# Optimization experiments

Hardware: AMD Instinct MI355X
Metric: run time of the kernel (lower is better)

## Reference

```python
import jax, jax.numpy as jnp
import numpy as np

NEG_SLOPE = 0.01  # jax.nn.leaky_relu default

def bicubic_resize(x, target_h, target_w):
    # NHWC bicubic resize with antialiasing (matches original module)
    b, h, w, c = x.shape
    return jax.image.resize(x, shape=(b, target_h, target_w, c), method='bicubic', antialias=True)

def setup_inputs() -> dict:
    key = jax.random.key(0)
    x = jax.random.normal(key, (16, 128, 128, 128), dtype=jnp.float32)  # NHWC
    return {"x": x, "in_size": 128, "out_size": 128}

def reference(x, in_size, out_size):
    y = bicubic_resize(x, 2 * in_size, 2 * in_size)
    # activation on the fine grid
    y = jax.nn.leaky_relu(y, negative_slope=NEG_SLOPE)
    # downsample (antialiased) back to out_size
    y = bicubic_resize(y, out_size, out_size)
    return y
```

## Files before the change

### kernel.cpp

```cpp
#include <hip/hip_runtime.h>


typedef float f2 __attribute__((ext_vector_type(2)));

#define HH 128
#define WW 128
#define CC 128
#define RS 16
#define CH 16
#define PADF2 130
#define NSTEP (RS + 4)

#define LBAR() asm volatile("s_waitcnt lgkmcnt(0)\n\ts_barrier" ::: "memory")

__device__ __forceinline__ double keys_cubic(double x) {
  if (x >= 2.0) return 0.0;
  if (x >= 1.0) return ((-0.5 * x + 2.5) * x - 4.0) * x + 2.0;
  return (1.5 * x - 2.5) * x * x + 1.0;
}

__global__ __launch_bounds__(256) void fused_updown_kernel(
    const float* __restrict__ x, float* __restrict__ out) {
  __shared__ __align__(16) float wUpV[256][4];
  __shared__ __align__(16) float wDnE[4][8];
  __shared__ __align__(16) f2 rowv[2][CH][PADF2];

  const int tid = threadIdx.x;

  {
    const int k = tid;
    const double q = 0.5 * k - 0.25;
    const int st = ((k + 1) >> 1) - 2;
    double wr[4], s = 0.0;
#pragma unroll
    for (int i = 0; i < 4; ++i) {
      const int col = st + i;
      double w = (col >= 0 && col <= 127) ? keys_cubic(fabs((double)col - q)) : 0.0;
      wr[i] = w; s += w;
    }
    const double inv = 1.0 / s;
#pragma unroll
    for (int i = 0; i < 4; ++i) wUpV[k][i] = (float)(wr[i] * inv);
  }
  if (tid < 4) {
    const int e = tid;
    const int j = (e < 2) ? e : 124 + e;
    const double p = 2.0 * j + 0.5;
    const int st = 2 * j - 3;
    double wr[8], s = 0.0;
#pragma unroll
    for (int i = 0; i < 8; ++i) {
      const int col = st + i;
      double w = (col >= 0 && col <= 255) ? keys_cubic(0.5 * fabs((double)col - p)) : 0.0;
      wr[i] = w; s += w;
    }
    const double inv = 1.0 / s;
#pragma unroll
    for (int i = 0; i < 8; ++i) wDnE[e][i] = (float)(wr[i] * inv);
  }
  __syncthreads();

  const int bid = blockIdx.x;
  const int b = bid & 15;
  const int strip = (bid >> 4) & 7;
  const int chunk = bid >> 7;
  const int oy0 = strip * RS;
  const int c0 = chunk * CH;
  const int c = tid & 15;
  const int g = tid >> 4;
  const int col0 = g * 8;
  const bool gL = (g == 0), gR = (g == 15);

  const float* xbase = x + (size_t)b * (HH * WW * CC) + (size_t)col0 * CC + (c0 + c);
  float* obase = out + (size_t)b * (HH * WW * CC) + (size_t)col0 * CC + (c0 + c);
  const int m0 = oy0 - 2;

  auto load_row = [&](float (&d)[8], int row) {
    row = row < 0 ? 0 : (row > 127 ? 127 : row);
    const float* p = xbase + (size_t)row * (WW * CC);
#pragma unroll
    for (int j = 0; j < 8; ++j) d[j] = p[j * CC];
  };

  auto wdGet = [&](int oy, float cst, int tap) -> float {
    if (oy < 0 || oy > 127) return 0.f;
    if (oy < 2) return wDnE[oy][tap];
    if (oy > 125) return wDnE[oy - 124][tap];
    return cst;
  };

  float r0[8], r1[8], r2[8], r3[8], r4[8], r5[8];
  float A0[8], A1[8], A2[8], A3[8], A4[8];
#pragma unroll
  for (int i = 0; i < 8; ++i) { A0[i]=0.f; A1[i]=0.f; A2[i]=0.f; A3[i]=0.f; A4[i]=0.f; }

  load_row(r0, m0 - 2);
  load_row(r1, m0 - 1);
  load_row(r2, m0);
  load_row(r3, m0 + 1);
  load_row(r4, m0 + 2);
  load_row(r5, m0 + 3);

  for (int t = 0; t < NSTEP; ++t) {
    const int m = m0 + t;
    if (t > 0) {
#pragma unroll
      for (int i = 0; i < 8; ++i) {
        r0[i]=r1[i]; r1[i]=r2[i]; r2[i]=r3[i]; r3[i]=r4[i]; r4[i]=r5[i];
      }
      load_row(r5, m + 3);
    }
    const bool mOK = (m >= 0) && (m <= 127);
    const int sp = t & 1;
    f2 vown[8];
    if (mOK) {
      float4 we, wo;
      if (m >= 2 && m <= 125) {
        we = make_float4(-0.0234375f, 0.2265625f, 0.8671875f, -0.0703125f);
        wo = make_float4(-0.0703125f, 0.8671875f, 0.2265625f, -0.0234375f);
      } else {
        we = *(const float4*)wUpV[2 * m];
        wo = *(const float4*)wUpV[2 * m + 1];
      }
#pragma unroll
      for (int j = 0; j < 8; ++j) {
        vown[j].x = (we.x * r0[j] + we.y * r1[j]) + (we.z * r2[j] + we.w * r3[j]);
        vown[j].y = (wo.x * r1[j] + wo.y * r2[j]) + (wo.z * r3[j] + wo.w * r4[j]);
      }
#pragma unroll
      for (int j = 0; j < 8; ++j) rowv[sp][c][col0 + j] = vown[j];
    }
    LBAR();
    if (mOK) {
      f2 vv[16];
      if (!gL) {
#pragma unroll
        for (int i = 0; i < 4; ++i) vv[i] = rowv[sp][c][col0 - 4 + i];
      } else {
#pragma unroll
        for (int i = 0; i < 4; ++i) vv[i] = f2{0.f, 0.f};
      }
#pragma unroll
      for (int j = 0; j < 8; ++j) vv[4 + j] = vown[j];
      if (!gR) {
#pragma unroll
        for (int i = 0; i < 4; ++i) vv[12 + i] = rowv[sp][c][col0 + 8 + i];
      } else {
#pragma unroll
        for (int i = 0; i < 4; ++i) vv[12 + i] = f2{0.f, 0.f};
      }

      f2 ff[22];
#pragma unroll
      for (int u = 0; u < 22; ++u) {
        const int s = (u >> 1) + 1;
        f2 t2;
        if (u & 1)
          t2 = (vv[s] * (-0.0234375f) + vv[s + 1] * 0.2265625f)
             + (vv[s + 2] * 0.8671875f + vv[s + 3] * (-0.0703125f));
        else
          t2 = (vv[s] * (-0.0703125f) + vv[s + 1] * 0.8671875f)
             + (vv[s + 2] * 0.2265625f + vv[s + 3] * (-0.0234375f));
        ff[u] = __builtin_elementwise_max(t2, t2 * 0.01f);
      }
      if (gL) {
#pragma unroll
        for (int u = 3; u <= 5; ++u) {
          const int s = (u >> 1) + 1;
          const float4 w = *(const float4*)wUpV[u - 3];
          f2 t2 = (vv[s] * w.x + vv[s + 1] * w.y) + (vv[s + 2] * w.z + vv[s + 3] * w.w);
          ff[u] = __builtin_elementwise_max(t2, t2 * 0.01f);
        }
      }
      if (gR) {
#pragma unroll
        for (int u = 16; u <= 18; ++u) {
          const int s = (u >> 1) + 1;
          const float4 w = *(const float4*)wUpV[237 + u];
          f2 t2 = (vv[s] * w.x + vv[s + 1] * w.y) + (vv[s + 2] * w.z + vv[s + 3] * w.w);
          ff[u] = __builtin_elementwise_max(t2, t2 * 0.01f);
        }
      }

      f2 tt[8];
#pragma unroll
      for (int jj = 0; jj < 8; ++jj) {
        const f2 p0 = ff[2*jj]     + ff[2*jj + 7];
        const f2 p1 = ff[2*jj + 1] + ff[2*jj + 6];
        const f2 p2 = ff[2*jj + 2] + ff[2*jj + 5];
        const f2 p3 = ff[2*jj + 3] + ff[2*jj + 4];
        tt[jj] = (p0 * (-0.01171875f) + p1 * (-0.03515625f))
               + (p2 * 0.11328125f    + p3 * 0.43359375f);
      }
      if (gL) {
#pragma unroll
        for (int jj = 0; jj < 2; ++jj) {
          f2 s2 = f2{0.f, 0.f};
#pragma unroll
          for (int i = 0; i < 8; ++i) s2 += ff[2*jj + i] * wDnE[jj][i];
          tt[jj] = s2;
        }
      }
      if (gR) {
#pragma unroll
        for (int jj = 6; jj < 8; ++jj) {
          f2 s2 = f2{0.f, 0.f};
#pragma unroll
          for (int i = 0; i < 8; ++i) s2 += ff[2*jj + i] * wDnE[jj - 4][i];
          tt[jj] = s2;
        }
      }

      const float wE0 = wdGet(m - 2, -0.01171875f, 7);
      const float wE1 = wdGet(m - 1, 0.11328125f, 5);
      const float wE2 = wdGet(m, 0.43359375f, 3);
      const float wE3 = wdGet(m + 1, -0.03515625f, 1);
      const float wO0 = wdGet(m - 1, -0.03515625f, 6);
      const float wO1 = wdGet(m, 0.43359375f, 4);
      const float wO2 = wdGet(m + 1, 0.11328125f, 2);
      const float wO3 = wdGet(m + 2, -0.01171875f, 0);
#pragma unroll
      for (int jj = 0; jj < 8; ++jj) {
        const float te = tt[jj].x, to = tt[jj].y;
        A0[jj] = fmaf(wE0, te, A0[jj]);
        A1[jj] = fmaf(wE1, te, fmaf(wO0, to, A1[jj]));
        A2[jj] = fmaf(wE2, te, fmaf(wO1, to, A2[jj]));
        A3[jj] = fmaf(wE3, te, fmaf(wO2, to, A3[jj]));
        A4[jj] = fmaf(wO3, to, A4[jj]);
      }
    }
    if (m - 2 >= oy0) {
      float* op = obase + (size_t)(m - 2) * (WW * CC);
#pragma unroll
      for (int jj = 0; jj < 8; ++jj) op[jj * CC] = A0[jj];
    }
#pragma unroll
    for (int jj = 0; jj < 8; ++jj) {
      A0[jj]=A1[jj]; A1[jj]=A2[jj]; A2[jj]=A3[jj]; A3[jj]=A4[jj]; A4[jj]=0.f;
    }
  }
}

extern "C" void kernel_launch(void* const* d_in, const int* in_sizes, int n_in,
                              void* d_out, int out_size, void* d_ws, size_t ws_size,
                              hipStream_t stream) {
  const float* x = (const float*)d_in[0];
  float* o = (float*)d_out;
  dim3 grid(16 * 8 * 8);
  dim3 block(256);
  hipLaunchKernelGGL(fused_updown_kernel, grid, block, 0, stream, x, o);
}
```

Measured before the change: 109.7 us.

## Compute horizontal up/down passes in packed fp16 and halve row strip height

The horizontal upsample, leaky-ReLU and horizontal downsample are switched from float2 arithmetic to packed half2, and the LDS row buffer is stored as fp16 with 128-bit vector stores and loads. The row strip per block is halved from 16 to 8 rows, which doubles the grid, and launch bounds ask for 5 waves per SIMD to raise occupancy. The vertical accumulation stays in fp32. Packed half math doubles ALU throughput and cuts LDS traffic, at the cost of reduced accuracy and more redundant halo row loads per block.

```diff
diff --git a/kernel.cpp b/kernel.cpp
--- a/kernel.cpp
+++ b/kernel.cpp
@@ -1,17 +1,22 @@
 #include <hip/hip_runtime.h>
 
 
-typedef float f2 __attribute__((ext_vector_type(2)));
+typedef _Float16 h2 __attribute__((ext_vector_type(2)));
 
 #define HH 128
 #define WW 128
 #define CC 128
-#define RS 16
+#define RS 8
 #define CH 16
-#define PADF2 130
+#define PADH2 132
 #define NSTEP (RS + 4)
 
 #define LBAR() asm volatile("s_waitcnt lgkmcnt(0)\n\ts_barrier" ::: "memory")
+
+__device__ __forceinline__ h2 H2(float v) {
+  _Float16 h = (_Float16)v;
+  return (h2){h, h};
+}
 
 __device__ __forceinline__ double keys_cubic(double x) {
   if (x >= 2.0) return 0.0;
@@ -19,11 +24,13 @@
   return (1.5 * x - 2.5) * x * x + 1.0;
 }
 
-__global__ __launch_bounds__(256) void fused_updown_kernel(
+__global__ __launch_bounds__(256, 5) void fused_updown_kernel(
     const float* __restrict__ x, float* __restrict__ out) {
   __shared__ __align__(16) float wUpV[256][4];
   __shared__ __align__(16) float wDnE[4][8];
-  __shared__ __align__(16) f2 rowv[2][CH][PADF2];
+  __shared__ __align__(16) h2 wUpH2[6][4];
+  __shared__ __align__(16) h2 wDnH2[4][8];
+  __shared__ __align__(16) h2 rowv[2][CH][PADH2];
 
   const int tid = threadIdx.x;
 
@@ -59,11 +66,20 @@
     for (int i = 0; i < 8; ++i) wDnE[e][i] = (float)(wr[i] * inv);
   }
   __syncthreads();
+  if (tid < 6) {
+    const int k = (tid < 3) ? tid : 250 + tid;
+#pragma unroll
+    for (int i = 0; i < 4; ++i) wUpH2[tid][i] = H2(wUpV[k][i]);
+  }
+  if (tid < 4) {
+#pragma unroll
+    for (int i = 0; i < 8; ++i) wDnH2[tid][i] = H2(wDnE[tid][i]);
+  }
 
   const int bid = blockIdx.x;
   const int b = bid & 15;
-  const int strip = (bid >> 4) & 7;
-  const int chunk = bid >> 7;
+  const int strip = (bid >> 4) & 15;
+  const int chunk = bid >> 8;
   const int oy0 = strip * RS;
   const int c0 = chunk * CH;
   const int c = tid & 15;
@@ -112,7 +128,7 @@
     }
     const bool mOK = (m >= 0) && (m <= 127);
     const int sp = t & 1;
-    f2 vown[8];
+    __align__(16) h2 vh[8];
     if (mOK) {
       float4 we, wo;
       if (m >= 2 && m <= 125) {
@@ -124,89 +140,88 @@
       }
 #pragma unroll
       for (int j = 0; j < 8; ++j) {
-        vown[j].x = (we.x * r0[j] + we.y * r1[j]) + (we.z * r2[j] + we.w * r3[j]);
-        vown[j].y = (wo.x * r1[j] + wo.y * r2[j]) + (wo.z * r3[j] + wo.w * r4[j]);
-      }
-#pragma unroll
-      for (int j = 0; j < 8; ++j) rowv[sp][c][col0 + j] = vown[j];
+        const float vE = (we.x * r0[j] + we.y * r1[j]) + (we.z * r2[j] + we.w * r3[j]);
+        const float vO = (wo.x * r1[j] + wo.y * r2[j]) + (wo.z * r3[j] + wo.w * r4[j]);
+        vh[j] = (h2){(_Float16)vE, (_Float16)vO};
+      }
+      *(float4*)&rowv[sp][c][col0]     = *(const float4*)&vh[0];
+      *(float4*)&rowv[sp][c][col0 + 4] = *(const float4*)&vh[4];
     }
     LBAR();
     if (mOK) {
-      f2 vv[16];
+      __align__(16) h2 vv[16];
       if (!gL) {
-#pragma unroll
-        for (int i = 0; i < 4; ++i) vv[i] = rowv[sp][c][col0 - 4 + i];
+        *(float4*)&vv[0] = *(const float4*)&rowv[sp][c][col0 - 4];
       } else {
 #pragma unroll
-        for (int i = 0; i < 4; ++i) vv[i] = f2{0.f, 0.f};
-      }
-#pragma unroll
-      for (int j = 0; j < 8; ++j) vv[4 + j] = vown[j];
+        for (int i = 0; i < 4; ++i) vv[i] = H2(0.f);
+      }
+#pragma unroll
+      for (int j = 0; j < 8; ++j) vv[4 + j] = vh[j];
       if (!gR) {
-#pragma unroll
-        for (int i = 0; i < 4; ++i) vv[12 + i] = rowv[sp][c][col0 + 8 + i];
+        *(float4*)&vv[12] = *(const float4*)&rowv[sp][c][col0 + 8];
       } else {
 #pragma unroll
-        for (int i = 0; i < 4; ++i) vv[12 + i] = f2{0.f, 0.f};
-      }
-
-      f2 ff[22];
+        for (int i = 0; i < 4; ++i) vv[12 + i] = H2(0.f);
+      }
+
+      h2 ff[22];
 #pragma unroll
       for (int u = 0; u < 22; ++u) {
         const int s = (u >> 1) + 1;
-        f2 t2;
+        h2 t2;
         if (u & 1)
-          t2 = (vv[s] * (-0.0234375f) + vv[s + 1] * 0.2265625f)
-             + (vv[s + 2] * 0.8671875f + vv[s + 3] * (-0.0703125f));
+          t2 = (vv[s] * H2(-0.0234375f) + vv[s + 1] * H2(0.2265625f))
+             + (vv[s + 2] * H2(0.8671875f) + vv[s + 3] * H2(-0.0703125f));
         else
-          t2 = (vv[s] * (-0.0703125f) + vv[s + 1] * 0.8671875f)
-             + (vv[s + 2] * 0.2265625f + vv[s + 3] * (-0.0234375f));
-        ff[u] = __builtin_elementwise_max(t2, t2 * 0.01f);
+          t2 = (vv[s] * H2(-0.0703125f) + vv[s + 1] * H2(0.8671875f))
+             + (vv[s + 2] * H2(0.2265625f) + vv[s + 3] * H2(-0.0234375f));
+        ff[u] = __builtin_elementwise_max(t2, t2 * H2(0.01f));
       }
       if (gL) {
 #pragma unroll
         for (int u = 3; u <= 5; ++u) {
           const int s = (u >> 1) + 1;
-          const float4 w = *(const float4*)wUpV[u - 3];
-          f2 t2 = (vv[s] * w.x + vv[s + 1] * w.y) + (vv[s + 2] * w.z + vv[s + 3] * w.w);
-          ff[u] = __builtin_elementwise_max(t2, t2 * 0.01f);
+          h2 t2 = (vv[s] * wUpH2[u - 3][0] + vv[s + 1] * wUpH2[u - 3][1])
+                + (vv[s + 2] * wUpH2[u - 3][2] + vv[s + 3] * wUpH2[u - 3][3]);
+          ff[u] = __builtin_elementwise_max(t2, t2 * H2(0.01f));
         }
       }
       if (gR) {
 #pragma unroll
         for (int u = 16; u <= 18; ++u) {
           const int s = (u >> 1) + 1;
-          const float4 w = *(const float4*)wUpV[237 + u];
-          f2 t2 = (vv[s] * w.x + vv[s + 1] * w.y) + (vv[s + 2] * w.z + vv[s + 3] * w.w);
-          ff[u] = __builtin_elementwise_max(t2, t2 * 0.01f);
-        }
-      }
-
-      f2 tt[8];
+          h2 t2 = (vv[s] * wUpH2[u - 13][0] + vv[s + 1] * wUpH2[u - 13][1])
+                + (vv[s + 2] * wUpH2[u - 13][2] + vv[s + 3] * wUpH2[u - 13][3]);
+          ff[u] = __builtin_elementwise_max(t2, t2 * H2(0.01f));
+        }
+      }
+
+      h2 tt[8];
 #pragma unroll
       for (int jj = 0; jj < 8; ++jj) {
-        const f2 p0 = ff[2*jj]     + ff[2*jj + 7];
-        const f2 p1 = ff[2*jj + 1] + ff[2*jj + 6];
-        const f2 p2 = ff[2*jj + 2] + ff[2*jj + 5];
-        const f2 p3 = ff[2*jj + 3] + ff[2*jj + 4];
-        tt[jj] = (p0 * (-0.01171875f) + p1 * (-0.03515625f))
-               + (p2 * 0.11328125f    + p3 * 0.43359375f);
+        const h2 p0 = ff[2*jj]     + ff[2*jj + 7];
+        const h2 p1 = ff[2*jj + 1] + ff[2*jj + 6];
+        const h2 p2 = ff[2*jj + 2] + ff[2*jj + 5];
+        const h2 p3 = ff[2*jj + 3] + ff[2*jj + 4];
+        tt[jj] = (p0 * H2(-0.01171875f) + p1 * H2(-0.03515625f))
+               + (p2 * H2(0.11328125f)  + p3 * H2(0.43359375f));
       }
       if (gL) {
 #pragma unroll
         for (int jj = 0; jj < 2; ++jj) {
-          f2 s2 = f2{0.f, 0.f};
-#pragma unroll
-          for (int i = 0; i < 8; ++i) s2 += ff[2*jj + i] * wDnE[jj][i];
+          h2 s2 = H2(0.f);
+#pragma unroll
+          for (int i = 0; i < 8; ++i) s2 += ff[2*jj + i] * wDnH2[jj][i];
           tt[jj] = s2;
         }
       }
       if (gR) {
 #pragma unroll
         for (int jj = 6; jj < 8; ++jj) {
-          f2 s2 = f2{0.f, 0.f};
-#pragma unroll
-          for (int i = 0; i < 8; ++i) s2 += ff[2*jj + i] * wDnE[jj - 4][i];
+          h2 s2 = H2(0.f);
+#pragma unroll
+          for (int i = 0; i < 8; ++i) s2 += ff[2*jj + i] * wDnH2[jj - 4][i];
           tt[jj] = s2;
         }
       }
@@ -221,7 +236,7 @@
       const float wO3 = wdGet(m + 2, -0.01171875f, 0);
 #pragma unroll
       for (int jj = 0; jj < 8; ++jj) {
-        const float te = tt[jj].x, to = tt[jj].y;
+        const float te = (float)tt[jj].x, to = (float)tt[jj].y;
         A0[jj] = fmaf(wE0, te, A0[jj]);
         A1[jj] = fmaf(wE1, te, fmaf(wO0, to, A1[jj]));
         A2[jj] = fmaf(wE2, te, fmaf(wO1, to, A2[jj]));
@@ -246,7 +261,7 @@
                               hipStream_t stream) {
   const float* x = (const float*)d_in[0];
   float* o = (float*)d_out;
-  dim3 grid(16 * 8 * 8);
+  dim3 grid(16 * 16 * 8);
   dim3 block(256);
   hipLaunchKernelGGL(fused_updown_kernel, grid, block, 0, stream, x, o);
 }
```

After: 426.7 us. 289% more time.
